# Optimization experiments

Measured on AMD Instinct MI355X. Metric: run time of the kernel, lower is better.

## Reference

```python
import jax, jax.numpy as jnp
import numpy as np

EPS = 1e-6  # mmdet bbox_overlaps eps


def _nearest_bev(boxes7):
    # boxes7: [N, 7] = (x, y, z, dx, dy, dz, yaw). LiDARInstance3DBoxes.nearest_bev:
    # limit yaw to [-pi/2, pi/2) via limit_period(yaw, 0.5, pi); if |yaw| > pi/4 swap dx/dy,
    # then return axis-aligned (x1, y1, x2, y2).
    x, y = boxes7[:, 0], boxes7[:, 1]
    dx, dy = boxes7[:, 3], boxes7[:, 4]
    yaw = boxes7[:, 6]
    pi = jnp.float32(np.pi)
    normed = jnp.abs(yaw - jnp.floor(yaw / pi + 0.5) * pi)
    swap = normed > pi / 4
    w = jnp.where(swap, dy, dx)
    h = jnp.where(swap, dx, dy)
    return jnp.stack([x - w / 2, y - h / 2, x + w / 2, y + h / 2], axis=-1)


def _pairwise_iou(b):
    # b: [N, 4] x1y1x2y2 -> [N, N] IoU (mmdet bbox_overlaps, mode='iou')
    area = (b[:, 2] - b[:, 0]) * (b[:, 3] - b[:, 1])
    lt = jnp.maximum(b[:, None, :2], b[None, :, :2])
    rb = jnp.minimum(b[:, None, 2:], b[None, :, 2:])
    wh = jnp.clip(rb - lt, 0.0)
    inter = wh[..., 0] * wh[..., 1]
    union = jnp.maximum(area[:, None] + area[None, :] - inter, EPS)
    return inter / union


def setup_inputs() -> dict:
    key = jax.random.key(0)
    k1, k2, k3, k4, k5, k6 = jax.random.split(key, 6)
    B, A, C, H, W, box_dim = 2, 2, 10, 32, 32, 7
    N = H * W * A
    scores = jax.random.normal(k1, (B, A * C, H, W), jnp.float32)
    bbox_preds = jax.random.normal(k2, (B, A * box_dim, H, W), jnp.float32)
    pp_params = jax.random.normal(k3, (B, C * 3, H, W), jnp.float32)
    centers = jax.random.uniform(k4, (B, N, 3), jnp.float32, 0.0, 50.0)
    sizes = jax.random.uniform(k5, (B, N, 3), jnp.float32, 1.0, 5.0)
    yaw = jax.random.uniform(k6, (B, N, 1), jnp.float32, -np.pi, np.pi)
    decoded = jnp.concatenate([centers, sizes, yaw], axis=-1)  # [B, N, 7]
    return {"scores": scores, "bbox_preds": bbox_preds, "pp_params": pp_params, "decoded": decoded}


def reference(scores, bbox_preds, pp_params, decoded):
    B, AC, H, W = scores.shape
    N = decoded.shape[1]
    A = N // (H * W)
    C = AC // A
    # flatten_scores: (B,A,C,H,W) -> (B,H,W,A,C) -> (B, HWA, C)
    sc_f = scores.reshape(B, A, C, H, W).transpose(0, 3, 4, 1, 2).reshape(B, N, C)
    # flatten_pp: (B,C,3,H,W) -> (B,H,W,C,3), broadcast over A -> (B, HWA, C, 3)
    pp_hw = pp_params.reshape(B, C, 3, H, W).transpose(0, 3, 4, 1, 2)  # [B,H,W,C,3]
    pp_f = jnp.broadcast_to(pp_hw[:, :, :, None, :, :], (B, H, W, A, C, 3)).reshape(B, N, C, 3)
    # per-batch BEV IoU matrices
    bev = jax.vmap(_nearest_bev)(decoded[..., :7])        # [B, N, 4]
    iou = jax.vmap(_pairwise_iou)(bev)                    # [B, N, N]
    # per-class outer-product bias + row softmax + matmul with column softmax of scores
    p0 = pp_f[..., 0]                                     # [B, N, C]
    p1 = pp_f[..., 1]                                     # [B, N, C]
    bias = p0[:, :, None, :] * p1[:, None, :, :]          # [B, N, N, C]
    weight = jax.nn.softmax(iou[..., None] + bias, axis=2)  # softmax over keys (dim=1 of NxN)
    sm_sc = jax.nn.softmax(sc_f, axis=1)                  # softmax over N per class
    new_sc = jnp.einsum('bnmc,bmc->bnc', weight, sm_sc)   # [B, N, C]
    # un-flatten back to level layout: (B,H,W,A,C) -> (B, A*C, H, W)
    out_scores = new_sc.reshape(B, H, W, A, C).transpose(0, 3, 4, 1, 2).reshape(B, A * C, H, W)
    return out_scores, bbox_preds, pp_params
```

## Files before the change

### kernel.cpp

```cpp
#include <hip/hip_runtime.h>
#include <math.h>

#define Bz 2
#define Az 2
#define Cz 10
#define HWz 1024
#define Nz 2048
#define ACHW (Az*Cz*HWz)
#define NBBOX (Bz*Az*7*HWz)
#define NPP   (Bz*Cz*3*HWz)
#define EPSf 1e-6f
#define LOG2E 1.4426950408889634f

#if __has_builtin(__builtin_amdgcn_exp2f)
#define EXP2F(x) __builtin_amdgcn_exp2f(x)
#else
#define EXP2F(x) exp2f(x)
#endif
#if __has_builtin(__builtin_amdgcn_rcpf)
#define RCPF(x) __builtin_amdgcn_rcpf(x)
#else
#define RCPF(x) (1.0f/(x))
#endif

static __device__ __forceinline__ unsigned short f2bf(float x) {
    unsigned u = __builtin_bit_cast(unsigned, x);
    unsigned r = (u + 0x7fffu + ((u >> 16) & 1u)) >> 16;
    return (unsigned short)r;
}

static __device__ __forceinline__ float iou_e(float nx1,float ny1,float nx2,float ny2,float ar,
                                              float mx1,float my1,float mx2,float my2,float am) {
    float xx1 = fmaxf(nx1, mx1), yy1 = fmaxf(ny1, my1);
    float xx2 = fminf(nx2, mx2), yy2 = fminf(ny2, my2);
    float iw = fmaxf(xx2 - xx1, 0.f), ih = fmaxf(yy2 - yy1, 0.f);
    float inter = iw * ih;
    float uni = fmaxf(ar + am - inter, EPSf);
    return EXP2F(inter * LOG2E * RCPF(uni));
}


__global__ __launch_bounds__(256) void k_pre(const float* __restrict__ scores,
                                             const float* __restrict__ bbox,
                                             const float* __restrict__ pp,
                                             const float* __restrict__ dec,
                                             float* __restrict__ out,
                                             float2* __restrict__ LT,
                                             float2* __restrict__ RB,
                                             uint2* __restrict__ GPQ2) {
    int blk = blockIdx.x;
    int tid = threadIdx.x;
    __shared__ float red[256];

    if (blk < 240) {
        int i = blk * 256 + tid;
        if (i < NBBOX) out[Bz*ACHW + i] = bbox[i];
        if (i < NPP)   out[Bz*ACHW + NBBOX + i] = pp[i];
        return;
    }
    if (blk < 256) {
        int i = (blk - 240) * 256 + tid;
        const float* d = dec + i*7;
        float x = d[0], y = d[1], dx = d[3], dy = d[4], yaw = d[6];
        const float PI = 3.14159265358979323846f;
        float normed = fabsf(yaw - floorf(yaw/PI + 0.5f) * PI);
        bool swp = normed > PI * 0.25f;
        float w = swp ? dy : dx;
        float h = swp ? dx : dy;
        LT[i] = make_float2(x - 0.5f*w, y - 0.5f*h);
        RB[i] = make_float2(x + 0.5f*w, y + 0.5f*h);
        return;
    }
    int bc = blk - 256;
    int b = bc / Cz, c = bc % Cz;
    const float* sbase = scores + b*ACHW;
    float vals[Nz/256];
    float mx = -INFINITY;
    #pragma unroll
    for (int j = 0; j < Nz/256; j++) {
        int n = tid + j*256;
        int a = n & 1, hw = n >> 1;
        float v = sbase[(a*Cz + c)*HWz + hw];
        vals[j] = v;
        mx = fmaxf(mx, v);
    }
    red[tid] = mx; __syncthreads();
    for (int s = 128; s > 0; s >>= 1) {
        if (tid < s) red[tid] = fmaxf(red[tid], red[tid+s]);
        __syncthreads();
    }
    mx = red[0]; __syncthreads();
    float sum = 0.f;
    #pragma unroll
    for (int j = 0; j < Nz/256; j++) {
        vals[j] = EXP2F((vals[j] - mx) * LOG2E);
        sum += vals[j];
    }
    red[tid] = sum; __syncthreads();
    for (int s = 128; s > 0; s >>= 1) {
        if (tid < s) red[tid] += red[tid+s];
        __syncthreads();
    }
    float inv = 1.f / red[0];
    const float* p1base = pp + b*Cz*3*HWz + (c*3 + 1)*HWz;
    uint2* gp = GPQ2 + (size_t)b*HWz*Cz;
    #pragma unroll
    for (int j = 0; j < Nz/256; j++) {
        __syncthreads();
        red[tid] = vals[j] * inv;
        __syncthreads();
        if (tid < 128) {
            int hm = (j << 7) + tid;
            float q0 = red[2*tid], q1 = red[2*tid + 1];
            unsigned qq = (unsigned)f2bf(q0) | ((unsigned)f2bf(q1) << 16);
            float p1 = p1base[hm] * LOG2E;
            gp[hm*Cz + c] = make_uint2(__builtin_bit_cast(unsigned, p1), qq);
        }
    }
}

__global__ __launch_bounds__(256, 2) void k_main(const float4* __restrict__ LT4,
                                                 const float4* __restrict__ RB4,
                                                 const uint2* __restrict__ GPQ2,
                                                 const float* __restrict__ pp,
                                                 float* __restrict__ P) {
    __shared__ __align__(16) char smem[40960];
    float4* SLT = (float4*)smem;
    float4* SRB = SLT + 64;
    uint2*  SPQ = (uint2*)(SRB + 64);
    float*  RED = (float*)smem;

    int tid = threadIdx.x;
    int wave = tid >> 6, lane = tid & 63;
    int bid = blockIdx.x;
    int b = bid >> 8;
    int r = bid & 255;
    int g = r >> 4, sp = r & 15;
    int hbase = sp << 6;

    const float4* LTb = LT4 + (b << 10);
    const float4* RBb = RB4 + (b << 10);
    const uint2*  Qb  = GPQ2 + (size_t)b*HWz*Cz + (size_t)hbase*Cz;

    if (tid < 64)       SLT[tid] = LTb[hbase + tid];
    else if (tid < 128) SRB[tid - 64] = RBb[hbase + tid - 64];
    #pragma unroll
    for (int i = tid; i < 640; i += 256) SPQ[i] = Qb[i];

    int hn = (g << 6) + lane;
    float4 bx = LTb[hn], by = RBb[hn];
    float ar0 = (by.x - bx.x) * (by.y - bx.y);
    float ar1 = (by.z - bx.z) * (by.w - bx.w);
    float p0[Cz];
    const float* p0base = pp + b*(Cz*3*HWz) + hn;
    #pragma unroll
    for (int c = 0; c < Cz; c++) p0[c] = p0base[c * 3 * HWz];

    float l0[Cz], l1[Cz], a0[Cz], a1[Cz];
    #pragma unroll
    for (int c = 0; c < Cz; c++) { l0[c]=0.f; l1[c]=0.f; a0[c]=0.f; a1[c]=0.f; }

    __syncthreads();

    int j0 = wave << 4;
    #pragma unroll 4
    for (int i = 0; i < 16; i++) {
        int j = j0 + i;
        float4 bl = SLT[j];
        float4 br = SRB[j];
        float am0 = (br.x - bl.x) * (br.y - bl.y);
        float am1 = (br.z - bl.z) * (br.w - bl.w);
        float E00 = iou_e(bx.x,bx.y,by.x,by.y,ar0, bl.x,bl.y,br.x,br.y,am0);
        float E01 = iou_e(bx.x,bx.y,by.x,by.y,ar0, bl.z,bl.w,br.z,br.w,am1);
        float E10 = iou_e(bx.z,bx.w,by.z,by.w,ar1, bl.x,bl.y,br.x,br.y,am0);
        float E11 = iou_e(bx.z,bx.w,by.z,by.w,ar1, bl.z,bl.w,br.z,br.w,am1);
        float S0 = E00 + E01, S1 = E10 + E11;
        const uint2* pqrow = SPQ + j*Cz;
        #pragma unroll
        for (int c = 0; c < Cz; c++) {
            uint2 pq = pqrow[c];
            float p1 = __builtin_bit_cast(float, pq.x);
            float q0 = __builtin_bit_cast(float, pq.y << 16);
            float q1 = __builtin_bit_cast(float, pq.y & 0xffff0000u);
            float F = EXP2F(p0[c] * p1);
            l0[c] = fmaf(F, S0, l0[c]);
            l1[c] = fmaf(F, S1, l1[c]);
            float t0 = fmaf(E01, q1, E00 * q0);
            float t1 = fmaf(E11, q1, E10 * q0);
            a0[c] = fmaf(F, t0, a0[c]);
            a1[c] = fmaf(F, t1, a1[c]);
        }
    }

    __syncthreads();
    float* rw = RED + (wave*64 + lane)*40;
    #pragma unroll
    for (int c = 0; c < Cz; c++) {
        rw[c]      = l0[c];
        rw[10 + c] = l1[c];
        rw[20 + c] = a0[c];
        rw[30 + c] = a1[c];
    }
    __syncthreads();

    int vg = tid >> 6, ln = tid & 63;
    float* Pb = P + (size_t)bid * 2560;
    #pragma unroll
    for (int k = 0; k < 10; k++) {
        int v = vg + (k << 2);
        float s = RED[(0*64+ln)*40 + v] + RED[(1*64+ln)*40 + v]
                + RED[(2*64+ln)*40 + v] + RED[(3*64+ln)*40 + v];
        Pb[v*64 + ln] = s;
    }
}

__global__ __launch_bounds__(256) void k_red(const float* __restrict__ P,
                                             float* __restrict__ out) {
    int bg = blockIdx.x;
    int b = bg >> 4, g = bg & 15;
    const float* Pb = P + (size_t)bg * 16 * 2560;
    int tid = threadIdx.x;
    #pragma unroll
    for (int k = 0; k < 5; k++) {
        int pos = tid + (k << 8);
        int v2 = pos >> 6, ln = pos & 63;
        float l = 0.f, a = 0.f;
        #pragma unroll
        for (int sp = 0; sp < 16; sp++) {
            const float* q = Pb + sp*2560;
            l += q[pos];
            a += q[1280 + pos];
        }
        int row = v2 / 10, c = v2 % 10;
        out[b*ACHW + (row*Cz + c)*HWz + (g << 6) + ln] = a * RCPF(l);
    }
}

extern "C" void kernel_launch(void* const* d_in, const int* in_sizes, int n_in,
                              void* d_out, int out_size, void* d_ws, size_t ws_size,
                              hipStream_t stream) {
    const float* scores = (const float*)d_in[0];
    const float* bbox   = (const float*)d_in[1];
    const float* pp     = (const float*)d_in[2];
    const float* dec    = (const float*)d_in[3];
    float* out = (float*)d_out;

    float2* LT = (float2*)d_ws;
    float2* RB = LT + (size_t)Bz*Nz;
    uint2*  PQ = (uint2*)(RB + (size_t)Bz*Nz);
    float*  P  = (float*)(PQ + (size_t)Bz*HWz*Cz);

    hipLaunchKernelGGL(k_pre,  dim3(276), dim3(256), 0, stream,
                       scores, bbox, pp, dec, out, LT, RB, PQ);
    hipLaunchKernelGGL(k_main, dim3(512), dim3(256), 0, stream,
                       (const float4*)LT, (const float4*)RB, PQ, pp, P);
    hipLaunchKernelGGL(k_red,  dim3(32),  dim3(256), 0, stream, P, out);
}
```

Before: 85.41 us.

## Split key range finer and reduce partial sums with shared and global atomics

Result: slower. 139.6 us (+63.5%).

```diff
diff --git a/kernel.cpp b/kernel.cpp
--- a/kernel.cpp
+++ b/kernel.cpp
@@ -11,6 +11,7 @@
 #define NPP   (Bz*Cz*3*HWz)
 #define EPSf 1e-6f
 #define LOG2E 1.4426950408889634f
+#define NACC (Bz*16*2560)
 
 #if __has_builtin(__builtin_amdgcn_exp2f)
 #define EXP2F(x) __builtin_amdgcn_exp2f(x)
@@ -47,7 +48,8 @@
                                              float* __restrict__ out,
                                              float2* __restrict__ LT,
                                              float2* __restrict__ RB,
-                                             uint2* __restrict__ GPQ2) {
+                                             uint2* __restrict__ GPQ2,
+                                             float* __restrict__ A) {
     int blk = blockIdx.x;
     int tid = threadIdx.x;
     __shared__ float red[256];
@@ -71,6 +73,11 @@
         RB[i] = make_float2(x + 0.5f*w, y + 0.5f*h);
         return;
     }
+    if (blk >= 276) {
+        float4* A4 = (float4*)A;
+        A4[(blk - 276) * 256 + tid] = make_float4(0.f, 0.f, 0.f, 0.f);
+        return;
+    }
     int bc = blk - 256;
     int b = bc / Cz, c = bc % Cz;
     const float* sbase = scores + b*ACHW;
@@ -119,33 +126,33 @@
     }
 }
 
-__global__ __launch_bounds__(256, 2) void k_main(const float4* __restrict__ LT4,
+__global__ __launch_bounds__(256, 4) void k_main(const float4* __restrict__ LT4,
                                                  const float4* __restrict__ RB4,
                                                  const uint2* __restrict__ GPQ2,
                                                  const float* __restrict__ pp,
-                                                 float* __restrict__ P) {
-    __shared__ __align__(16) char smem[40960];
-    float4* SLT = (float4*)smem;
-    float4* SRB = SLT + 64;
-    uint2*  SPQ = (uint2*)(SRB + 64);
-    float*  RED = (float*)smem;
+                                                 float* __restrict__ A) {
+    __shared__ __align__(16) float4 SLT[32];
+    __shared__ __align__(16) float4 SRB[32];
+    __shared__ __align__(16) uint2  SPQ[320];
+    __shared__ float RED[2560];
 
     int tid = threadIdx.x;
     int wave = tid >> 6, lane = tid & 63;
     int bid = blockIdx.x;
-    int b = bid >> 8;
-    int r = bid & 255;
-    int g = r >> 4, sp = r & 15;
-    int hbase = sp << 6;
+    int b = bid >> 9;
+    int r = bid & 511;
+    int g = r >> 5, sp = r & 31;
+    int hbase = sp << 5;
 
     const float4* LTb = LT4 + (b << 10);
     const float4* RBb = RB4 + (b << 10);
     const uint2*  Qb  = GPQ2 + (size_t)b*HWz*Cz + (size_t)hbase*Cz;
 
-    if (tid < 64)       SLT[tid] = LTb[hbase + tid];
-    else if (tid < 128) SRB[tid - 64] = RBb[hbase + tid - 64];
-    #pragma unroll
-    for (int i = tid; i < 640; i += 256) SPQ[i] = Qb[i];
+    if (tid < 32)       SLT[tid] = LTb[hbase + tid];
+    else if (tid < 64)  SRB[tid - 32] = RBb[hbase + tid - 32];
+    for (int i = tid; i < 320; i += 256) SPQ[i] = Qb[i];
+    #pragma unroll
+    for (int k = 0; k < 10; k++) RED[tid + (k << 8)] = 0.f;
 
     int hn = (g << 6) + lane;
     float4 bx = LTb[hn], by = RBb[hn];
@@ -162,12 +169,15 @@
 
     __syncthreads();
 
-    int j0 = wave << 4;
-    #pragma unroll 4
-    for (int i = 0; i < 16; i++) {
-        int j = j0 + i;
-        float4 bl = SLT[j];
-        float4 br = SRB[j];
+    int j = wave << 3;
+    float4 bl = SLT[j], br = SRB[j];
+    #pragma unroll 2
+    for (int i = 0; i < 8; i++) {
+        const uint4* row4 = (const uint4*)(SPQ + j*Cz);
+        uint4 q01 = row4[0], q23 = row4[1], q45 = row4[2], q67 = row4[3], q89 = row4[4];
+        float4 nbl, nbr;
+        if (i < 7) { nbl = SLT[j+1]; nbr = SRB[j+1]; }
+
         float am0 = (br.x - bl.x) * (br.y - bl.y);
         float am1 = (br.z - bl.z) * (br.w - bl.w);
         float E00 = iou_e(bx.x,bx.y,by.x,by.y,ar0, bl.x,bl.y,br.x,br.y,am0);
@@ -175,13 +185,14 @@
         float E10 = iou_e(bx.z,bx.w,by.z,by.w,ar1, bl.x,bl.y,br.x,br.y,am0);
         float E11 = iou_e(bx.z,bx.w,by.z,by.w,ar1, bl.z,bl.w,br.z,br.w,am1);
         float S0 = E00 + E01, S1 = E10 + E11;
-        const uint2* pqrow = SPQ + j*Cz;
+
+        unsigned pqx[Cz] = {q01.x, q01.z, q23.x, q23.z, q45.x, q45.z, q67.x, q67.z, q89.x, q89.z};
+        unsigned pqy[Cz] = {q01.y, q01.w, q23.y, q23.w, q45.y, q45.w, q67.y, q67.w, q89.y, q89.w};
         #pragma unroll
         for (int c = 0; c < Cz; c++) {
-            uint2 pq = pqrow[c];
-            float p1 = __builtin_bit_cast(float, pq.x);
-            float q0 = __builtin_bit_cast(float, pq.y << 16);
-            float q1 = __builtin_bit_cast(float, pq.y & 0xffff0000u);
+            float p1 = __builtin_bit_cast(float, pqx[c]);
+            float q0 = __builtin_bit_cast(float, pqy[c] << 16);
+            float q1 = __builtin_bit_cast(float, pqy[c] & 0xffff0000u);
             float F = EXP2F(p0[c] * p1);
             l0[c] = fmaf(F, S0, l0[c]);
             l1[c] = fmaf(F, S1, l1[c]);
@@ -190,47 +201,39 @@
             a0[c] = fmaf(F, t0, a0[c]);
             a1[c] = fmaf(F, t1, a1[c]);
         }
+        bl = nbl; br = nbr; j++;
     }
 
     __syncthreads();
-    float* rw = RED + (wave*64 + lane)*40;
     #pragma unroll
     for (int c = 0; c < Cz; c++) {
-        rw[c]      = l0[c];
-        rw[10 + c] = l1[c];
-        rw[20 + c] = a0[c];
-        rw[30 + c] = a1[c];
+        atomicAdd(&RED[(c      ) * 64 + lane], l0[c]);
+        atomicAdd(&RED[(10 + c) * 64 + lane], l1[c]);
+        atomicAdd(&RED[(20 + c) * 64 + lane], a0[c]);
+        atomicAdd(&RED[(30 + c) * 64 + lane], a1[c]);
     }
     __syncthreads();
 
-    int vg = tid >> 6, ln = tid & 63;
-    float* Pb = P + (size_t)bid * 2560;
+    float* Ab = A + (size_t)(b*16 + g) * 2560;
     #pragma unroll
     for (int k = 0; k < 10; k++) {
-        int v = vg + (k << 2);
-        float s = RED[(0*64+ln)*40 + v] + RED[(1*64+ln)*40 + v]
-                + RED[(2*64+ln)*40 + v] + RED[(3*64+ln)*40 + v];
-        Pb[v*64 + ln] = s;
-    }
-}
-
-__global__ __launch_bounds__(256) void k_red(const float* __restrict__ P,
+        int u = tid + (k << 8);
+        atomicAdd(Ab + u, RED[u]);
+    }
+}
+
+__global__ __launch_bounds__(256) void k_fin(const float* __restrict__ A,
                                              float* __restrict__ out) {
     int bg = blockIdx.x;
     int b = bg >> 4, g = bg & 15;
-    const float* Pb = P + (size_t)bg * 16 * 2560;
+    const float* Ab = A + (size_t)bg * 2560;
     int tid = threadIdx.x;
     #pragma unroll
     for (int k = 0; k < 5; k++) {
         int pos = tid + (k << 8);
         int v2 = pos >> 6, ln = pos & 63;
-        float l = 0.f, a = 0.f;
-        #pragma unroll
-        for (int sp = 0; sp < 16; sp++) {
-            const float* q = Pb + sp*2560;
-            l += q[pos];
-            a += q[1280 + pos];
-        }
+        float l = Ab[pos];
+        float a = Ab[1280 + pos];
         int row = v2 / 10, c = v2 % 10;
         out[b*ACHW + (row*Cz + c)*HWz + (g << 6) + ln] = a * RCPF(l);
     }
@@ -248,11 +251,11 @@
     float2* LT = (float2*)d_ws;
     float2* RB = LT + (size_t)Bz*Nz;
     uint2*  PQ = (uint2*)(RB + (size_t)Bz*Nz);
-    float*  P  = (float*)(PQ + (size_t)Bz*HWz*Cz);
-
-    hipLaunchKernelGGL(k_pre,  dim3(276), dim3(256), 0, stream,
-                       scores, bbox, pp, dec, out, LT, RB, PQ);
-    hipLaunchKernelGGL(k_main, dim3(512), dim3(256), 0, stream,
-                       (const float4*)LT, (const float4*)RB, PQ, pp, P);
-    hipLaunchKernelGGL(k_red,  dim3(32),  dim3(256), 0, stream, P, out);
-}
+    float*  A  = (float*)(PQ + (size_t)Bz*HWz*Cz);
+
+    hipLaunchKernelGGL(k_pre,  dim3(356),  dim3(256), 0, stream,
+                       scores, bbox, pp, dec, out, LT, RB, PQ, A);
+    hipLaunchKernelGGL(k_main, dim3(1024), dim3(256), 0, stream,
+                       (const float4*)LT, (const float4*)RB, PQ, pp, A);
+    hipLaunchKernelGGL(k_fin,  dim3(32),   dim3(256), 0, stream, A, out);
+}
```

## Split key range finer, store fp32 score softmax, widen reduction grid

Applied to the files above, without the earlier changes.

Result: slower. 98.99 us (+15.9%).

```diff
diff --git a/kernel.cpp b/kernel.cpp
--- a/kernel.cpp
+++ b/kernel.cpp
@@ -23,12 +23,6 @@
 #define RCPF(x) (1.0f/(x))
 #endif
 
-static __device__ __forceinline__ unsigned short f2bf(float x) {
-    unsigned u = __builtin_bit_cast(unsigned, x);
-    unsigned r = (u + 0x7fffu + ((u >> 16) & 1u)) >> 16;
-    return (unsigned short)r;
-}
-
 static __device__ __forceinline__ float iou_e(float nx1,float ny1,float nx2,float ny2,float ar,
                                               float mx1,float my1,float mx2,float my2,float am) {
     float xx1 = fmaxf(nx1, mx1), yy1 = fmaxf(ny1, my1);
@@ -47,7 +41,7 @@
                                              float* __restrict__ out,
                                              float2* __restrict__ LT,
                                              float2* __restrict__ RB,
-                                             uint2* __restrict__ GPQ2) {
+                                             float4* __restrict__ GPQ4) {
     int blk = blockIdx.x;
     int tid = threadIdx.x;
     __shared__ float red[256];
@@ -103,7 +97,7 @@
     }
     float inv = 1.f / red[0];
     const float* p1base = pp + b*Cz*3*HWz + (c*3 + 1)*HWz;
-    uint2* gp = GPQ2 + (size_t)b*HWz*Cz;
+    float4* gp = GPQ4 + (size_t)b*HWz*Cz;
     #pragma unroll
     for (int j = 0; j < Nz/256; j++) {
         __syncthreads();
@@ -112,40 +106,38 @@
         if (tid < 128) {
             int hm = (j << 7) + tid;
             float q0 = red[2*tid], q1 = red[2*tid + 1];
-            unsigned qq = (unsigned)f2bf(q0) | ((unsigned)f2bf(q1) << 16);
             float p1 = p1base[hm] * LOG2E;
-            gp[hm*Cz + c] = make_uint2(__builtin_bit_cast(unsigned, p1), qq);
+            gp[hm*Cz + c] = make_float4(p1, q0, q1, 0.f);
         }
     }
 }
 
-__global__ __launch_bounds__(256, 2) void k_main(const float4* __restrict__ LT4,
+__global__ __launch_bounds__(256, 4) void k_main(const float4* __restrict__ LT4,
                                                  const float4* __restrict__ RB4,
-                                                 const uint2* __restrict__ GPQ2,
+                                                 const float4* __restrict__ GPQ4,
                                                  const float* __restrict__ pp,
                                                  float* __restrict__ P) {
     __shared__ __align__(16) char smem[40960];
-    float4* SLT = (float4*)smem;
-    float4* SRB = SLT + 64;
-    uint2*  SPQ = (uint2*)(SRB + 64);
-    float*  RED = (float*)smem;
+    float4* SLT  = (float4*)smem;
+    float4* SRB  = SLT + 32;
+    float4* SPQ4 = SRB + 32;
+    float*  RED  = (float*)smem;
 
     int tid = threadIdx.x;
     int wave = tid >> 6, lane = tid & 63;
     int bid = blockIdx.x;
-    int b = bid >> 8;
-    int r = bid & 255;
-    int g = r >> 4, sp = r & 15;
-    int hbase = sp << 6;
+    int b = bid >> 9;
+    int r = bid & 511;
+    int g = r >> 5, sp = r & 31;
+    int hbase = sp << 5;
 
     const float4* LTb = LT4 + (b << 10);
     const float4* RBb = RB4 + (b << 10);
-    const uint2*  Qb  = GPQ2 + (size_t)b*HWz*Cz + (size_t)hbase*Cz;
-
-    if (tid < 64)       SLT[tid] = LTb[hbase + tid];
-    else if (tid < 128) SRB[tid - 64] = RBb[hbase + tid - 64];
-    #pragma unroll
-    for (int i = tid; i < 640; i += 256) SPQ[i] = Qb[i];
+    const float4* Qb  = GPQ4 + (size_t)b*HWz*Cz + (size_t)hbase*Cz;
+
+    if (tid < 32)       SLT[tid] = LTb[hbase + tid];
+    else if (tid < 64)  SRB[tid - 32] = RBb[hbase + tid - 32];
+    for (int i = tid; i < 320; i += 256) SPQ4[i] = Qb[i];
 
     int hn = (g << 6) + lane;
     float4 bx = LTb[hn], by = RBb[hn];
@@ -162,10 +154,9 @@
 
     __syncthreads();
 
-    int j0 = wave << 4;
-    #pragma unroll 4
-    for (int i = 0; i < 16; i++) {
-        int j = j0 + i;
+    int j = wave << 3;
+    #pragma unroll 2
+    for (int i = 0; i < 8; i++, j++) {
         float4 bl = SLT[j];
         float4 br = SRB[j];
         float am0 = (br.x - bl.x) * (br.y - bl.y);
@@ -175,65 +166,60 @@
         float E10 = iou_e(bx.z,bx.w,by.z,by.w,ar1, bl.x,bl.y,br.x,br.y,am0);
         float E11 = iou_e(bx.z,bx.w,by.z,by.w,ar1, bl.z,bl.w,br.z,br.w,am1);
         float S0 = E00 + E01, S1 = E10 + E11;
-        const uint2* pqrow = SPQ + j*Cz;
+        const float4* pqrow = SPQ4 + j*Cz;
         #pragma unroll
         for (int c = 0; c < Cz; c++) {
-            uint2 pq = pqrow[c];
-            float p1 = __builtin_bit_cast(float, pq.x);
-            float q0 = __builtin_bit_cast(float, pq.y << 16);
-            float q1 = __builtin_bit_cast(float, pq.y & 0xffff0000u);
-            float F = EXP2F(p0[c] * p1);
+            float4 pq = pqrow[c];
+            float F = EXP2F(p0[c] * pq.x);
             l0[c] = fmaf(F, S0, l0[c]);
             l1[c] = fmaf(F, S1, l1[c]);
-            float t0 = fmaf(E01, q1, E00 * q0);
-            float t1 = fmaf(E11, q1, E10 * q0);
+            float t0 = fmaf(E01, pq.z, E00 * pq.y);
+            float t1 = fmaf(E11, pq.z, E10 * pq.y);
             a0[c] = fmaf(F, t0, a0[c]);
             a1[c] = fmaf(F, t1, a1[c]);
         }
     }
 
     __syncthreads();
-    float* rw = RED + (wave*64 + lane)*40;
-    #pragma unroll
-    for (int c = 0; c < Cz; c++) {
-        rw[c]      = l0[c];
-        rw[10 + c] = l1[c];
-        rw[20 + c] = a0[c];
-        rw[30 + c] = a1[c];
+    {
+        float* rw = RED + (wave << 6) + lane;
+        #pragma unroll
+        for (int c = 0; c < Cz; c++) {
+            rw[(c      ) << 8] = l0[c];
+            rw[(10 + c) << 8] = l1[c];
+            rw[(20 + c) << 8] = a0[c];
+            rw[(30 + c) << 8] = a1[c];
+        }
     }
     __syncthreads();
 
+    float* Pb = P + (size_t)bid * 2560;
     int vg = tid >> 6, ln = tid & 63;
-    float* Pb = P + (size_t)bid * 2560;
     #pragma unroll
     for (int k = 0; k < 10; k++) {
         int v = vg + (k << 2);
-        float s = RED[(0*64+ln)*40 + v] + RED[(1*64+ln)*40 + v]
-                + RED[(2*64+ln)*40 + v] + RED[(3*64+ln)*40 + v];
-        Pb[v*64 + ln] = s;
+        const float* rr = RED + (v << 8) + ln;
+        Pb[tid + (k << 8)] = rr[0] + rr[64] + rr[128] + rr[192];
     }
 }
 
 __global__ __launch_bounds__(256) void k_red(const float* __restrict__ P,
                                              float* __restrict__ out) {
-    int bg = blockIdx.x;
+    int bid = blockIdx.x;
+    int bg = bid / 5, f = bid % 5;
     int b = bg >> 4, g = bg & 15;
-    const float* Pb = P + (size_t)bg * 16 * 2560;
-    int tid = threadIdx.x;
-    #pragma unroll
-    for (int k = 0; k < 5; k++) {
-        int pos = tid + (k << 8);
-        int v2 = pos >> 6, ln = pos & 63;
-        float l = 0.f, a = 0.f;
-        #pragma unroll
-        for (int sp = 0; sp < 16; sp++) {
-            const float* q = Pb + sp*2560;
-            l += q[pos];
-            a += q[1280 + pos];
-        }
-        int row = v2 / 10, c = v2 % 10;
-        out[b*ACHW + (row*Cz + c)*HWz + (g << 6) + ln] = a * RCPF(l);
-    }
+    const float* Pb = P + (size_t)(b*512 + g*32) * 2560;
+    int pos = f*256 + threadIdx.x;
+    float l = 0.f, a = 0.f;
+    #pragma unroll
+    for (int sp = 0; sp < 32; sp++) {
+        const float* q = Pb + (size_t)sp*2560;
+        l += q[pos];
+        a += q[1280 + pos];
+    }
+    int v2 = pos >> 6, ln = pos & 63;
+    int row = v2 / 10, c = v2 % 10;
+    out[b*ACHW + (row*Cz + c)*HWz + (g << 6) + ln] = a * RCPF(l);
 }
 
 extern "C" void kernel_launch(void* const* d_in, const int* in_sizes, int n_in,
@@ -247,12 +233,12 @@
 
     float2* LT = (float2*)d_ws;
     float2* RB = LT + (size_t)Bz*Nz;
-    uint2*  PQ = (uint2*)(RB + (size_t)Bz*Nz);
+    float4* PQ = (float4*)(RB + (size_t)Bz*Nz);
     float*  P  = (float*)(PQ + (size_t)Bz*HWz*Cz);
 
-    hipLaunchKernelGGL(k_pre,  dim3(276), dim3(256), 0, stream,
+    hipLaunchKernelGGL(k_pre,  dim3(276),  dim3(256), 0, stream,
                        scores, bbox, pp, dec, out, LT, RB, PQ);
-    hipLaunchKernelGGL(k_main, dim3(512), dim3(256), 0, stream,
+    hipLaunchKernelGGL(k_main, dim3(1024), dim3(256), 0, stream,
                        (const float4*)LT, (const float4*)RB, PQ, pp, P);
-    hipLaunchKernelGGL(k_red,  dim3(32),  dim3(256), 0, stream, P, out);
-}
+    hipLaunchKernelGGL(k_red,  dim3(160),  dim3(256), 0, stream, P, out);
+}
```
